# Performance work log

Hardware: AMD Instinct MI355X
Metric: run time of the kernel (lower is better)

## Reference

```python
import jax, jax.numpy as jnp
import numpy as np

K_HOPS = 2  # SGConv K = nlayers


def setup_inputs() -> dict:
    key = jax.random.key(0)
    k1, k2, k3 = jax.random.split(key, 3)
    N, E, F, C = 100000, 1600000, 128, 40
    x = jax.random.normal(k1, (N, F), dtype=jnp.float32)
    edge_index = jax.random.randint(k2, (2, E), 0, N, dtype=jnp.int64)
    W = jax.random.normal(k3, (C, F), dtype=jnp.float32) * (1.0 / np.sqrt(F))
    b = jnp.zeros((C,), dtype=jnp.float32)
    return {"x": x, "edge_index": edge_index, "W": W, "b": b}


def reference(x, edge_index, W, b):
    # SGConv: K hops of GCN-normalized propagation (with self-loops), then Linear.
    N = x.shape[0]
    loop = jnp.arange(N, dtype=edge_index.dtype)
    src = jnp.concatenate([edge_index[0], loop])  # message source
    dst = jnp.concatenate([edge_index[1], loop])  # aggregation target
    w = jnp.ones(src.shape[0], dtype=x.dtype)     # edge_weight=None -> 1, self-loop fill=1
    deg = jax.ops.segment_sum(w, dst, num_segments=N)  # in-degree incl. self-loop (>=1)
    dinv = jax.lax.rsqrt(deg)
    norm = dinv[src] * w * dinv[dst]              # D^{-1/2} A D^{-1/2}
    h = x
    for _ in range(K_HOPS):
        h = jax.ops.segment_sum(norm[:, None] * h[src], dst, num_segments=N)
    return h @ W.T + b
```

## Files before the change

### kernel.cpp

```cpp
#include <hip/hip_runtime.h>
#include <hip/hip_fp16.h>
#include <cstdint>

#define CDIM 40
#define FDIM 128
#define BIN_SHIFT 8
#define BIN_SZ (1 << BIN_SHIFT)
#define CHUNK 4096
#define STAGE_CAP 8192

typedef _Float16 f16x8 __attribute__((ext_vector_type(8)));
typedef float f32x4 __attribute__((ext_vector_type(4)));

static __device__ __forceinline__ long long load_idx(const void* p, int is64, long long i) {
    if (is64) return ((const long long*)p)[i];
    return (long long)((const int*)p)[i];
}

static __device__ __forceinline__ unsigned packh2(float a, float b) {
    __half2 h;
    h.x = __float2half(a);
    h.y = __float2half(b);
    return *(unsigned*)&h;
}

static __device__ __forceinline__ void addv4(float* acc, uint4 v) {
    const __half2* h = (const __half2*)&v;
    float2 f0 = __half22float2(h[0]);
    float2 f1 = __half22float2(h[1]);
    float2 f2 = __half22float2(h[2]);
    float2 f3 = __half22float2(h[3]);
    acc[0] += f0.x; acc[1] += f0.y; acc[2] += f1.x; acc[3] += f1.y;
    acc[4] += f2.x; acc[5] += f2.y; acc[6] += f3.x; acc[7] += f3.y;
}

static __device__ __forceinline__ f16x8 cvt8(float4 a, float4 b) {
    f16x8 r;
    r[0] = (_Float16)a.x; r[1] = (_Float16)a.y; r[2] = (_Float16)a.z; r[3] = (_Float16)a.w;
    r[4] = (_Float16)b.x; r[5] = (_Float16)b.y; r[6] = (_Float16)b.z; r[7] = (_Float16)b.w;
    return r;
}

__global__ void k_init(int* cursor, int nb, int capRec) {
    int i = blockIdx.x * blockDim.x + threadIdx.x;
    if (i < nb) cursor[i] = i * capRec;
}

__global__ __launch_bounds__(256) void kA3(const void* ei, long long E,
                                           int nb, int* __restrict__ cursor,
                                           unsigned* __restrict__ binned) {
    __shared__ unsigned lval[CHUNK];
    __shared__ unsigned short lbin[CHUNK];
    __shared__ int lcnt[512];
    __shared__ int lbase[512];
    __shared__ int lflag;
    int tid = threadIdx.x;
    if (tid == 0) lflag = 1;
    for (int i = tid; i < nb; i += 256) lcnt[i] = 0;
    __syncthreads();
    {
        const unsigned* w = (const unsigned*)ei;
        int nscan = (int)((2 * E < 4096) ? (2 * E) : 4096);
        for (int k = 1 + 2 * tid; k < nscan; k += 512)
            if (w[k] != 0u) lflag = 0;
    }
    __syncthreads();
    int is64 = lflag;
    long long base = (long long)blockIdx.x * CHUNK;
    int nk = (int)min((long long)CHUNK, E - base);
    for (int k = tid; k < nk; k += 256) {
        long long e = base + k;
        int s = (int)load_idx(ei, is64, e);
        int d = (int)load_idx(ei, is64, E + e);
        int bin = d >> BIN_SHIFT;
        lval[k] = (unsigned)s | ((unsigned)(d & (BIN_SZ - 1)) << 17);
        lbin[k] = (unsigned short)bin;
        atomicAdd(&lcnt[bin], 1);
    }
    __syncthreads();
    for (int i = tid; i < nb; i += 256) {
        int c = lcnt[i];
        lbase[i] = c ? atomicAdd(&cursor[i], c) : 0;
        lcnt[i] = 0;
    }
    __syncthreads();
    for (int k = tid; k < nk; k += 256) {
        int bin = lbin[k];
        int loc = atomicAdd(&lcnt[bin], 1);
        binned[lbase[bin] + loc] = lval[k];
    }
}

__global__ __launch_bounds__(256) void kB(const unsigned* __restrict__ binned,
                                          const int* __restrict__ cursor,
                                          int capRec, int capC,
                                          int2* __restrict__ meta,
                                          float* __restrict__ dinv,
                                          int* __restrict__ cursorG,
                                          int* __restrict__ csr, int N) {
    __shared__ int lcnt[BIN_SZ];
    __shared__ int lexcl[BIN_SZ];
    __shared__ int ls[256];
    __shared__ int dh[64];
    __shared__ int tot;
    __shared__ int stage[STAGE_CAP];
    int b = blockIdx.x, tid = threadIdx.x;
    int node0 = b << BIN_SHIFT;
    int nn = min(BIN_SZ, N - node0);
    int recBase = b * capRec;
    int csrBase = b * capC;
    int nedges = cursor[b] - recBase;

    lcnt[tid] = 0;
    if (tid < 64) dh[tid] = 0;
    __syncthreads();
    for (int t = tid; t < nedges; t += 256)
        atomicAdd(&lcnt[(binned[recBase + t] >> 17) & (BIN_SZ - 1)], 1);
    __syncthreads();
    int myc = lcnt[tid];
    int psz = (myc + 3) & ~3;
    ls[tid] = psz;
    __syncthreads();
    for (int off = 1; off < 256; off <<= 1) {
        int t = (tid >= off) ? ls[tid - off] : 0;
        __syncthreads();
        ls[tid] += t;
        __syncthreads();
    }
    int ex = ls[tid] - psz;
    lexcl[tid] = ex;
    if (tid == 255) tot = ls[255];
    if (tid < nn) {
        dinv[node0 + tid] = rsqrtf(1.0f + (float)myc);
        atomicAdd(&dh[min(myc, 63)], 1);
    }
    __syncthreads();
    int total = tot;
    int dv = (tid < 64) ? dh[tid] : 0;
    ls[tid] = dv;
    __syncthreads();
    for (int off = 1; off < 64; off <<= 1) {
        int t = (tid >= off) ? ls[tid - off] : 0;
        __syncthreads();
        ls[tid] += t;
        __syncthreads();
    }
    if (tid < 64) dh[tid] = ls[tid] - dv;
    __syncthreads();
    if (tid < nn) {
        int pos = atomicAdd(&dh[min(myc, 63)], 1);
        int2 mi;
        mi.x = csrBase + ex;
        mi.y = (node0 + tid) | (myc << 17);
        meta[node0 + pos] = mi;
    }
    __syncthreads();
    lcnt[tid] = ex;
    __syncthreads();
    if (total <= STAGE_CAP) {
        for (int t = tid; t < total; t += 256) stage[t] = N;
        __syncthreads();
        for (int t = tid; t < nedges; t += 256) {
            unsigned v = binned[recBase + t];
            int src = (int)(v & 0x1FFFFu);
            int dl  = (int)((v >> 17) & (BIN_SZ - 1));
            int p = atomicAdd(&lcnt[dl], 1);
            stage[p] = src;
        }
        __syncthreads();
        const int4* sp = (const int4*)stage;
        int4* cp = (int4*)(csr + csrBase);
        for (int t = tid; t < (total >> 2); t += 256) cp[t] = sp[t];
    } else {
        if (tid < nn) cursorG[node0 + tid] = csrBase + ex;
        __syncthreads();
        for (int t = tid; t < nedges; t += 256) {
            unsigned v = binned[recBase + t];
            int src = (int)(v & 0x1FFFFu);
            int dl  = (int)((v >> 17) & (BIN_SZ - 1));
            int p = atomicAdd(&cursorG[node0 + dl], 1);
            csr[p] = src;
        }
        if (tid < nn)
            for (int k = myc; k < psz; ++k) csr[csrBase + ex + k] = N;
    }
}

__global__ __launch_bounds__(256) void k_gemm(const float* __restrict__ x,
                                              const float* __restrict__ W,
                                              const float* __restrict__ dinv,
                                              __half* __restrict__ gA,
                                              __half* __restrict__ gB, int N) {
    if (blockIdx.x == 0 && threadIdx.x < 20) {
        if (threadIdx.x < 16) ((unsigned*)(gA + (size_t)N * 32))[threadIdx.x] = 0u;
        else                  ((unsigned*)(gB + (size_t)N * 8))[threadIdx.x - 16] = 0u;
    }
    int wave = threadIdx.x >> 6;
    int lane = threadIdx.x & 63;
    int m = lane & 15;
    int quad = lane >> 4;
    f16x8 bfrag[3][4];
#pragma unroll
    for (int t = 0; t < 3; ++t) {
        int c = t * 16 + m;
#pragma unroll
        for (int q = 0; q < 4; ++q) {
            if (c < CDIM) {
                const float* wp = W + (size_t)c * FDIM + q * 32 + quad * 8;
                float4 w0 = *(const float4*)wp;
                float4 w1 = *(const float4*)(wp + 4);
                bfrag[t][q] = cvt8(w0, w1);
            } else {
                f16x8 z = {0, 0, 0, 0, 0, 0, 0, 0};
                bfrag[t][q] = z;
            }
        }
    }
#pragma unroll
    for (int i = 0; i < 4; ++i) {
        int nodebase = blockIdx.x * 256 + wave * 64 + i * 16;
        if (nodebase >= N) break;
        const float* xp = x + (size_t)(nodebase + m) * FDIM + quad * 8;
        f16x8 afrag[4];
#pragma unroll
        for (int q = 0; q < 4; ++q) {
            float4 x0 = *(const float4*)(xp + q * 32);
            float4 x1 = *(const float4*)(xp + q * 32 + 4);
            afrag[q] = cvt8(x0, x1);
        }
        f32x4 acc0 = {0, 0, 0, 0}, acc1 = {0, 0, 0, 0}, acc2 = {0, 0, 0, 0};
#pragma unroll
        for (int q = 0; q < 4; ++q) {
            acc0 = __builtin_amdgcn_mfma_f32_16x16x32_f16(afrag[q], bfrag[0][q], acc0, 0, 0, 0);
            acc1 = __builtin_amdgcn_mfma_f32_16x16x32_f16(afrag[q], bfrag[1][q], acc1, 0, 0, 0);
            acc2 = __builtin_amdgcn_mfma_f32_16x16x32_f16(afrag[q], bfrag[2][q], acc2, 0, 0, 0);
        }
        float4 dvv = *(const float4*)&dinv[nodebase + quad * 4];
        float ds[4] = {dvv.x, dvv.y, dvv.z, dvv.w};
#pragma unroll
        for (int r = 0; r < 4; ++r) {
            int node = nodebase + quad * 4 + r;
            gA[(size_t)node * 32 + m]      = __float2half(acc0[r] * ds[r]);
            gA[(size_t)node * 32 + 16 + m] = __float2half(acc1[r] * ds[r]);
            if (m < 8)
                gB[(size_t)node * 8 + m]   = __float2half(acc2[r] * ds[r]);
        }
    }
}

__global__ __launch_bounds__(256) void k_gather(const int2* __restrict__ meta,
                                                const int* __restrict__ csr,
                                                const __half* __restrict__ gA,
                                                const __half* __restrict__ gB,
                                                const float* __restrict__ b,
                                                __half* __restrict__ goA,
                                                __half* __restrict__ goB,
                                                float* __restrict__ outF,
                                                int N, int mode) {
    unsigned t = blockIdx.x * 256 + threadIdx.x;
    if (mode == 0 && t < 20) {
        if (t < 16) ((unsigned*)(goA + (size_t)N * 32))[t] = 0u;
        else        ((unsigned*)(goB + (size_t)N * 8))[t - 16] = 0u;
    }
    unsigned gidx = t / 5, c = t - gidx * 5;
    if (gidx >= (unsigned)N) return;
    int2 mi = meta[gidx];
    int j = mi.x;
    int node = mi.y & 0x1FFFF;
    int deg = mi.y >> 17;
    int end_pad = j + ((deg + 3) & ~3);
    const uint4* src;
    unsigned stride;
    if (c < 4) { src = (const uint4*)gA + c; stride = 4; }
    else       { src = (const uint4*)gB;     stride = 1; }
    float acc[8] = {0, 0, 0, 0, 0, 0, 0, 0};
    addv4(acc, src[(size_t)node * stride]);
    for (; j + 8 <= end_pad; j += 8) {
        int4 c0 = *(const int4*)&csr[j];
        int4 c1 = *(const int4*)&csr[j + 4];
        uint4 v0 = src[(size_t)c0.x * stride];
        uint4 v1 = src[(size_t)c0.y * stride];
        uint4 v2 = src[(size_t)c0.z * stride];
        uint4 v3 = src[(size_t)c0.w * stride];
        uint4 v4 = src[(size_t)c1.x * stride];
        uint4 v5 = src[(size_t)c1.y * stride];
        uint4 v6 = src[(size_t)c1.z * stride];
        uint4 v7 = src[(size_t)c1.w * stride];
        addv4(acc, v0); addv4(acc, v1); addv4(acc, v2); addv4(acc, v3);
        addv4(acc, v4); addv4(acc, v5); addv4(acc, v6); addv4(acc, v7);
    }
    if (j < end_pad) {
        int4 c0 = *(const int4*)&csr[j];
        uint4 v0 = src[(size_t)c0.x * stride];
        uint4 v1 = src[(size_t)c0.y * stride];
        uint4 v2 = src[(size_t)c0.z * stride];
        uint4 v3 = src[(size_t)c0.w * stride];
        addv4(acc, v0); addv4(acc, v1); addv4(acc, v2); addv4(acc, v3);
    }
    float d = rsqrtf(1.0f + (float)deg);
    if (mode == 0) {
        float s = d * d;
        uint4 o;
        o.x = packh2(acc[0] * s, acc[1] * s);
        o.y = packh2(acc[2] * s, acc[3] * s);
        o.z = packh2(acc[4] * s, acc[5] * s);
        o.w = packh2(acc[6] * s, acc[7] * s);
        if (c < 4) ((uint4*)goA)[(size_t)node * 4 + c] = o;
        else       ((uint4*)goB)[(size_t)node] = o;
    } else {
        float4 bv0 = ((const float4*)b)[2 * c];
        float4 bv1 = ((const float4*)b)[2 * c + 1];
        float4 o0, o1;
        o0.x = acc[0] * d + bv0.x;
        o0.y = acc[1] * d + bv0.y;
        o0.z = acc[2] * d + bv0.z;
        o0.w = acc[3] * d + bv0.w;
        o1.x = acc[4] * d + bv1.x;
        o1.y = acc[5] * d + bv1.y;
        o1.z = acc[6] * d + bv1.z;
        o1.w = acc[7] * d + bv1.w;
        ((float4*)outF)[(size_t)node * 10 + 2 * c]     = o0;
        ((float4*)outF)[(size_t)node * 10 + 2 * c + 1] = o1;
    }
}

static inline size_t align256(size_t v) { return (v + 255) & ~(size_t)255; }

extern "C" void kernel_launch(void* const* d_in, const int* in_sizes, int n_in,
                              void* d_out, int out_size, void* d_ws, size_t ws_size,
                              hipStream_t stream) {
    const float* x  = (const float*)d_in[0];
    const void*  ei = d_in[1];
    const float* W  = (const float*)d_in[2];
    const float* b  = (const float*)d_in[3];
    float* out = (float*)d_out;

    const int N = in_sizes[0] / FDIM;
    const long long E = (long long)in_sizes[1] / 2;

    const int nb     = (N + BIN_SZ - 1) >> BIN_SHIFT;
    const int nchunk = (int)((E + CHUNK - 1) / CHUNK);
    int capRec = (int)(E / nb) + 2048;
    if (capRec > STAGE_CAP) capRec = STAGE_CAP;
    int capC = (capRec + BIN_SZ * 3 + 1027) & ~3;

    char* wsb = (char*)d_ws;
    size_t off = 0;
    int*      cursor  = (int*)(wsb + off);      off = align256(off + (size_t)nb * 4);
    int*      cursorG = (int*)(wsb + off);      off = align256(off + (size_t)N * 4);
    int2*     meta    = (int2*)(wsb + off);     off = align256(off + (size_t)N * 8);
    float*    dinv    = (float*)(wsb + off);    off = align256(off + (size_t)N * 4);
    __half*   gA0     = (__half*)(wsb + off);   off = align256(off + (size_t)(N + 1) * 32 * 2);
    __half*   gB0     = (__half*)(wsb + off);   off = align256(off + (size_t)(N + 1) * 8 * 2);
    __half*   gA1     = (__half*)(wsb + off);   off = align256(off + (size_t)(N + 1) * 32 * 2);
    __half*   gB1     = (__half*)(wsb + off);   off = align256(off + (size_t)(N + 1) * 8 * 2);
    unsigned* binned  = (unsigned*)(wsb + off); off = align256(off + (size_t)nb * capRec * 4);
    int*      csr     = (int*)(wsb + off);      off = align256(off + (size_t)nb * capC * 4);

    const int B = 256;
    const int nbGE = (N + 255) / 256;
    const unsigned GT = 5u * (unsigned)N;
    const int nbGA = (int)((GT + B - 1) / B);

    k_init  <<<(nb + 255) / 256, 256, 0, stream>>>(cursor, nb, capRec);
    kA3     <<<nchunk, B, 0, stream>>>(ei, E, nb, cursor, binned);
    kB      <<<nb, B, 0, stream>>>(binned, cursor, capRec, capC, meta, dinv, cursorG, csr, N);
    k_gemm  <<<nbGE, B, 0, stream>>>(x, W, dinv, gA0, gB0, N);
    k_gather<<<nbGA, B, 0, stream>>>(meta, csr, gA0, gB0, b, gA1, gB1, nullptr, N, 0);
    k_gather<<<nbGA, B, 0, stream>>>(meta, csr, gA1, gB1, b, nullptr, nullptr, out, N, 1);
}
```

Measured before the change: 215.9 us.

## Fuse CSR build with GEMM projection and use wave-shuffle scans

Merges the per-bin CSR construction kernel with the x·Wᵀ MFMA projection kernel, so that each bin block computes dinv in shared memory and projects its own 256 nodes. This removes one launch and the global dinv round trip. The block-wide prefix scans are replaced with wave-level shuffle scans to cut barrier count, and the zeroing of padding rows moves into the init kernel. The cost is that the fused block carries the large shared-memory stage plus the GEMM register load, which may reduce occupancy.

```diff
diff --git a/kernel.cpp b/kernel.cpp
--- a/kernel.cpp
+++ b/kernel.cpp
@@ -41,9 +41,16 @@
     return r;
 }
 
-__global__ void k_init(int* cursor, int nb, int capRec) {
+__global__ void k_init(int* cursor, int nb, int capRec,
+                       __half* gA0, __half* gB0, __half* gA1, __half* gB1, int N) {
     int i = blockIdx.x * blockDim.x + threadIdx.x;
     if (i < nb) cursor[i] = i * capRec;
+    if (i < 40) {
+        if (i < 16)      ((unsigned*)(gA0 + (size_t)N * 32))[i] = 0u;
+        else if (i < 20) ((unsigned*)(gB0 + (size_t)N * 8))[i - 16] = 0u;
+        else if (i < 36) ((unsigned*)(gA1 + (size_t)N * 32))[i - 20] = 0u;
+        else             ((unsigned*)(gB1 + (size_t)N * 8))[i - 36] = 0u;
+    }
 }
 
 __global__ __launch_bounds__(256) void kA3(const void* ei, long long E,
@@ -91,20 +98,24 @@
     }
 }
 
-__global__ __launch_bounds__(256) void kB(const unsigned* __restrict__ binned,
-                                          const int* __restrict__ cursor,
-                                          int capRec, int capC,
-                                          int2* __restrict__ meta,
-                                          float* __restrict__ dinv,
-                                          int* __restrict__ cursorG,
-                                          int* __restrict__ csr, int N) {
+__global__ __launch_bounds__(256) void kBG(const unsigned* __restrict__ binned,
+                                           const int* __restrict__ cursor,
+                                           int capRec, int capC,
+                                           int2* __restrict__ meta,
+                                           int* __restrict__ cursorG,
+                                           int* __restrict__ csr,
+                                           const float* __restrict__ x,
+                                           const float* __restrict__ W,
+                                           __half* __restrict__ gA,
+                                           __half* __restrict__ gB, int N) {
     __shared__ int lcnt[BIN_SZ];
-    __shared__ int lexcl[BIN_SZ];
-    __shared__ int ls[256];
+    __shared__ int lsum[4];
     __shared__ int dh[64];
-    __shared__ int tot;
+    __shared__ float dinvL[BIN_SZ];
     __shared__ int stage[STAGE_CAP];
     int b = blockIdx.x, tid = threadIdx.x;
+    const int wid = tid >> 6;
+    const int lane = tid & 63;
     int node0 = b << BIN_SHIFT;
     int nn = min(BIN_SZ, N - node0);
     int recBase = b * capRec;
@@ -119,33 +130,35 @@
     __syncthreads();
     int myc = lcnt[tid];
     int psz = (myc + 3) & ~3;
-    ls[tid] = psz;
-    __syncthreads();
-    for (int off = 1; off < 256; off <<= 1) {
-        int t = (tid >= off) ? ls[tid - off] : 0;
-        __syncthreads();
-        ls[tid] += t;
-        __syncthreads();
-    }
-    int ex = ls[tid] - psz;
-    lexcl[tid] = ex;
-    if (tid == 255) tot = ls[255];
+    int incl = psz;
+#pragma unroll
+    for (int off = 1; off < 64; off <<= 1) {
+        int up = __shfl_up(incl, off, 64);
+        if (lane >= off) incl += up;
+    }
+    if (lane == 63) lsum[wid] = incl;
     if (tid < nn) {
-        dinv[node0 + tid] = rsqrtf(1.0f + (float)myc);
+        dinvL[tid] = rsqrtf(1.0f + (float)myc);
         atomicAdd(&dh[min(myc, 63)], 1);
-    }
-    __syncthreads();
-    int total = tot;
-    int dv = (tid < 64) ? dh[tid] : 0;
-    ls[tid] = dv;
-    __syncthreads();
-    for (int off = 1; off < 64; off <<= 1) {
-        int t = (tid >= off) ? ls[tid - off] : 0;
-        __syncthreads();
-        ls[tid] += t;
-        __syncthreads();
-    }
-    if (tid < 64) dh[tid] = ls[tid] - dv;
+    } else {
+        dinvL[tid] = 0.0f;
+    }
+    __syncthreads();
+    int woff = 0;
+#pragma unroll
+    for (int w = 0; w < 4; ++w) woff += (w < wid) ? lsum[w] : 0;
+    int ex = woff + incl - psz;
+    int total = lsum[0] + lsum[1] + lsum[2] + lsum[3];
+    if (wid == 0) {
+        int dv = dh[lane];
+        int di = dv;
+#pragma unroll
+        for (int off = 1; off < 64; off <<= 1) {
+            int up = __shfl_up(di, off, 64);
+            if (lane >= off) di += up;
+        }
+        dh[lane] = di - dv;
+    }
     __syncthreads();
     if (tid < nn) {
         int pos = atomicAdd(&dh[min(myc, 63)], 1);
@@ -184,21 +197,10 @@
         if (tid < nn)
             for (int k = myc; k < psz; ++k) csr[csrBase + ex + k] = N;
     }
-}
-
-__global__ __launch_bounds__(256) void k_gemm(const float* __restrict__ x,
-                                              const float* __restrict__ W,
-                                              const float* __restrict__ dinv,
-                                              __half* __restrict__ gA,
-                                              __half* __restrict__ gB, int N) {
-    if (blockIdx.x == 0 && threadIdx.x < 20) {
-        if (threadIdx.x < 16) ((unsigned*)(gA + (size_t)N * 32))[threadIdx.x] = 0u;
-        else                  ((unsigned*)(gB + (size_t)N * 8))[threadIdx.x - 16] = 0u;
-    }
-    int wave = threadIdx.x >> 6;
-    int lane = threadIdx.x & 63;
-    int m = lane & 15;
-    int quad = lane >> 4;
+    __syncthreads();
+
+    const int m = lane & 15;
+    const int quad = lane >> 4;
     f16x8 bfrag[3][4];
 #pragma unroll
     for (int t = 0; t < 3; ++t) {
@@ -218,7 +220,8 @@
     }
 #pragma unroll
     for (int i = 0; i < 4; ++i) {
-        int nodebase = blockIdx.x * 256 + wave * 64 + i * 16;
+        int lnode = wid * 64 + i * 16;
+        int nodebase = node0 + lnode;
         if (nodebase >= N) break;
         const float* xp = x + (size_t)(nodebase + m) * FDIM + quad * 8;
         f16x8 afrag[4];
@@ -235,8 +238,9 @@
             acc1 = __builtin_amdgcn_mfma_f32_16x16x32_f16(afrag[q], bfrag[1][q], acc1, 0, 0, 0);
             acc2 = __builtin_amdgcn_mfma_f32_16x16x32_f16(afrag[q], bfrag[2][q], acc2, 0, 0, 0);
         }
-        float4 dvv = *(const float4*)&dinv[nodebase + quad * 4];
-        float ds[4] = {dvv.x, dvv.y, dvv.z, dvv.w};
+        float ds[4];
+#pragma unroll
+        for (int r = 0; r < 4; ++r) ds[r] = dinvL[lnode + quad * 4 + r];
 #pragma unroll
         for (int r = 0; r < 4; ++r) {
             int node = nodebase + quad * 4 + r;
@@ -258,10 +262,6 @@
                                                 float* __restrict__ outF,
                                                 int N, int mode) {
     unsigned t = blockIdx.x * 256 + threadIdx.x;
-    if (mode == 0 && t < 20) {
-        if (t < 16) ((unsigned*)(goA + (size_t)N * 32))[t] = 0u;
-        else        ((unsigned*)(goB + (size_t)N * 8))[t - 16] = 0u;
-    }
     unsigned gidx = t / 5, c = t - gidx * 5;
     if (gidx >= (unsigned)N) return;
     int2 mi = meta[gidx];
@@ -349,7 +349,6 @@
     int*      cursor  = (int*)(wsb + off);      off = align256(off + (size_t)nb * 4);
     int*      cursorG = (int*)(wsb + off);      off = align256(off + (size_t)N * 4);
     int2*     meta    = (int2*)(wsb + off);     off = align256(off + (size_t)N * 8);
-    float*    dinv    = (float*)(wsb + off);    off = align256(off + (size_t)N * 4);
     __half*   gA0     = (__half*)(wsb + off);   off = align256(off + (size_t)(N + 1) * 32 * 2);
     __half*   gB0     = (__half*)(wsb + off);   off = align256(off + (size_t)(N + 1) * 8 * 2);
     __half*   gA1     = (__half*)(wsb + off);   off = align256(off + (size_t)(N + 1) * 32 * 2);
@@ -358,14 +357,13 @@
     int*      csr     = (int*)(wsb + off);      off = align256(off + (size_t)nb * capC * 4);
 
     const int B = 256;
-    const int nbGE = (N + 255) / 256;
     const unsigned GT = 5u * (unsigned)N;
     const int nbGA = (int)((GT + B - 1) / B);
 
-    k_init  <<<(nb + 255) / 256, 256, 0, stream>>>(cursor, nb, capRec);
+    k_init  <<<(nb + 255) / 256, 256, 0, stream>>>(cursor, nb, capRec, gA0, gB0, gA1, gB1, N);
     kA3     <<<nchunk, B, 0, stream>>>(ei, E, nb, cursor, binned);
-    kB      <<<nb, B, 0, stream>>>(binned, cursor, capRec, capC, meta, dinv, cursorG, csr, N);
-    k_gemm  <<<nbGE, B, 0, stream>>>(x, W, dinv, gA0, gB0, N);
+    kBG     <<<nb, B, 0, stream>>>(binned, cursor, capRec, capC, meta, cursorG, csr,
+                                   x, W, gA0, gB0, N);
     k_gather<<<nbGA, B, 0, stream>>>(meta, csr, gA0, gB0, b, gA1, gB1, nullptr, N, 0);
     k_gather<<<nbGA, B, 0, stream>>>(meta, csr, gA1, gB1, b, nullptr, nullptr, out, N, 1);
 }
```

Result: no change. 214.7 us (-0.5%).
